# Optimization experiments

Measured on AMD Instinct MI355X. Metric: run time of the kernel, lower is better.

The kernel has to match this reference:

```python
import jax, jax.numpy as jnp
import numpy as np

EPS = 1e-5

def layer_norm(x, gamma, beta):
    mu = jnp.mean(x, axis=-1, keepdims=True)
    var = jnp.mean(jnp.square(x - mu), axis=-1, keepdims=True)
    return (x - mu) * jax.lax.rsqrt(var + EPS) * gamma + beta

def setup_inputs() -> dict:
    key = jax.random.key(0)
    ks = jax.random.split(key, 12)
    B, C, W, H = 4, 512, 48, 48
    HEADS, DH = 8, 64
    INNER = HEADS * DH  # 512
    CTX_D, CTX_L = 768, 77
    x = jax.random.normal(ks[0], (B, C, W, H), dtype=jnp.float32)
    context = jax.random.normal(ks[1], (B, CTX_L, CTX_D), dtype=jnp.float32)
    inv = lambda d: 1.0 / np.sqrt(d)
    return {
        'x': x,
        'context': context,
        'norm_gamma': jnp.ones((C,), jnp.float32),
        'null_kv': jax.random.normal(ks[2], (2, DH), dtype=jnp.float32),
        'Wq': jax.random.normal(ks[3], (C, INNER), dtype=jnp.float32) * inv(C),
        'Wkv': jax.random.normal(ks[4], (C, 2 * DH), dtype=jnp.float32) * inv(C),
        'ctx_ln_g': jnp.ones((CTX_D,), jnp.float32),
        'ctx_ln_b': jnp.zeros((CTX_D,), jnp.float32),
        'Wctx': jax.random.normal(ks[5], (CTX_D, 2 * DH), dtype=jnp.float32) * inv(CTX_D),
        'bctx': jnp.zeros((2 * DH,), jnp.float32),
        'Wout': jax.random.normal(ks[6], (INNER, C), dtype=jnp.float32) * inv(INNER),
        'out_ln_g': jnp.ones((C,), jnp.float32),
    }

def reference(x, context, norm_gamma, null_kv, Wq, Wkv, ctx_ln_g, ctx_ln_b, Wctx, bctx, Wout, out_ln_g):
    b, c, w, h = x.shape
    heads = 8
    dh = Wkv.shape[-1] // 2
    scale = dh ** -0.5
    # b c w h -> b (w h) c
    x_flat = jnp.transpose(x.reshape(b, c, w * h), (0, 2, 1))  # [b, n, c]
    xn = layer_norm(x_flat, norm_gamma, 0.0)
    q = xn @ Wq  # [b, n, heads*dh]
    kv = xn @ Wkv
    k, v = kv[..., :dh], kv[..., dh:]  # [b, n, dh]
    n = w * h
    q = q.reshape(b, n, heads, dh).transpose(0, 2, 1, 3) * scale  # [b, h, n, d]
    # null kv: [2, dh] -> broadcast to [b, 1, dh] each
    nk = jnp.broadcast_to(null_kv[0], (b, 1, dh))
    nv = jnp.broadcast_to(null_kv[1], (b, 1, dh))
    k = jnp.concatenate([nk, k], axis=-2)
    v = jnp.concatenate([nv, v], axis=-2)
    # context kv
    ckv = layer_norm(context, ctx_ln_g, ctx_ln_b) @ Wctx + bctx
    ck, cv = ckv[..., :dh], ckv[..., dh:]
    k = jnp.concatenate([ck, k], axis=-2)  # [b, j, d]
    v = jnp.concatenate([cv, v], axis=-2)
    sim = jnp.einsum('bhid,bjd->bhij', q, k)  # [b, h, n, j]
    attn = jax.nn.softmax(sim, axis=-1)
    out = jnp.einsum('bhij,bjd->bhid', attn, v)
    out = out.transpose(0, 2, 1, 3).reshape(b, n, heads * dh)  # b n (h d)
    out = layer_norm(out @ Wout, out_ln_g, 0.0)
    y = x_flat + out  # [b, n, c]
    return jnp.transpose(y, (0, 2, 1)).reshape(b, c, w, h)
```

## Files before the change

### kernel.cpp

```cpp
#include <hip/hip_runtime.h>

typedef __attribute__((ext_vector_type(8))) short bf16x8;
typedef __attribute__((ext_vector_type(4))) float f32x4;

#define LPAD 2432
#define LKV  2382
#define NSEQ 2304
#define CDIM 512
#define LPSZ (4 * NSEQ * 8)

__device__ __forceinline__ unsigned short f2bf(float f) {
  unsigned int u = __builtin_bit_cast(unsigned int, f);
  u += 0x7fffu + ((u >> 16) & 1u);
  return (unsigned short)(u >> 16);
}
__device__ __forceinline__ float bf2f(unsigned short s) {
  unsigned int u = ((unsigned int)s) << 16;
  return __builtin_bit_cast(float, u);
}
__device__ __forceinline__ f32x4 MFMA(bf16x8 a, bf16x8 b, f32x4 c) {
  return __builtin_amdgcn_mfma_f32_16x16x32_bf16(a, b, c, 0, 0, 0);
}
__device__ __forceinline__ void stage16(const unsigned short* g, unsigned short* l) {
  __builtin_amdgcn_global_load_lds((const __attribute__((address_space(1))) void*)g,
                                   (__attribute__((address_space(3))) void*)l, 16, 0, 0);
}
__device__ __forceinline__ unsigned int cvtpk(float a, float b) {
  unsigned int r;
  asm("v_cvt_pk_bf16_f32 %0, %1, %2" : "=v"(r) : "v"(a), "v"(b));
  return r;
}
__device__ __forceinline__ int Fj(int j) {
  return (j & ~31) | ((j & 15) << 1) | ((j >> 4) & 1);
}

__device__ __forceinline__ void tr_tile(const float* __restrict__ in,
                                        unsigned short* __restrict__ out,
                                        int K, int N, int tk, int tn, int t) {
  __shared__ float T[32][33];
  int r = t >> 5, c = t & 31;
#pragma unroll
  for (int p = 0; p < 4; p++) {
    int rr = r + p * 8;
    T[rr][c] = in[(size_t)(tk * 32 + rr) * N + tn * 32 + c];
  }
  __syncthreads();
#pragma unroll
  for (int p = 0; p < 4; p++) {
    int rr = r + p * 8;
    out[(size_t)(tn * 32 + rr) * K + tk * 32 + c] = f2bf(T[c][rr]);
  }
}

__global__ void k_prep(const float* __restrict__ Wq, const float* __restrict__ Wkv,
                       const float* __restrict__ Wctx, const float* __restrict__ Wout,
                       unsigned short* __restrict__ WqT, unsigned short* __restrict__ WkvT,
                       unsigned short* __restrict__ WctxT, unsigned short* __restrict__ WoutT) {
  int bid = blockIdx.x, t = threadIdx.x;
  if (bid < 256) {
    tr_tile(Wq, WqT, 512, 512, bid >> 4, bid & 15, t);
  } else if (bid < 320) {
    int q = bid - 256;
    tr_tile(Wkv, WkvT, 512, 128, q >> 2, q & 3, t);
  } else if (bid < 416) {
    int q = bid - 320;
    tr_tile(Wctx, WctxT, 768, 128, q >> 2, q & 3, t);
  } else {
    int q = bid - 416;
    tr_tile(Wout, WoutT, 512, 512, q >> 4, q & 15, t);
  }
}

__global__ void k_ln1(const float* __restrict__ x, const float* __restrict__ g,
                      unsigned short* __restrict__ xn) {
  int b = blockIdx.y;
  int i0 = blockIdx.x * 32;
  int t = threadIdx.x;
  int ii = t & 31, ci = t >> 5;
  const float* xb = x + (size_t)b * CDIM * NSEQ;
  float s = 0.f, s2 = 0.f;
  for (int c = ci; c < CDIM; c += 8) {
    float v = xb[(size_t)c * NSEQ + i0 + ii];
    s += v; s2 += v * v;
  }
  __shared__ float ls[8][32], ls2[8][32];
  __shared__ float lmu[32], lrs[32];
  __shared__ float Lt[32][65];
  ls[ci][ii] = s; ls2[ci][ii] = s2;
  __syncthreads();
  if (t < 32) {
    float a = 0.f, a2 = 0.f;
    for (int q = 0; q < 8; q++) { a += ls[q][t]; a2 += ls2[q][t]; }
    float mu = a * (1.0f / 512.0f);
    float var = a2 * (1.0f / 512.0f) - mu * mu;
    lmu[t] = mu; lrs[t] = rsqrtf(var + 1e-5f);
  }
  __syncthreads();
  float mu = lmu[ii], rs = lrs[ii];
  int rr = t >> 3, cl0 = (t & 7) * 8;
  for (int cb = 0; cb < 8; cb++) {
#pragma unroll
    for (int e = 0; e < 8; e++) {
      int cl = ci + 8 * e;
      int c = cb * 64 + cl;
      float v = xb[(size_t)c * NSEQ + i0 + ii];
      Lt[ii][cl] = (v - mu) * rs * g[c];
    }
    __syncthreads();
    union { unsigned int w4[4]; uint4 u; } pk;
#pragma unroll
    for (int m = 0; m < 4; m++)
      pk.w4[m] = cvtpk(Lt[rr][cl0 + 2 * m], Lt[rr][cl0 + 2 * m + 1]);
    *reinterpret_cast<uint4*>(xn + (size_t)(b * NSEQ + i0 + rr) * CDIM + cb * 64 + cl0) = pk.u;
    __syncthreads();
  }
}

__global__ void k_ctx(const float* __restrict__ ctx, const float* __restrict__ g,
                      const float* __restrict__ be, const unsigned short* __restrict__ WctxT,
                      const float* __restrict__ bctx, const float* __restrict__ null_kv,
                      unsigned short* __restrict__ kb, unsigned short* __restrict__ vt) {
  int b = blockIdx.y, j = blockIdx.x;
  int t = threadIdx.x;
  if (j == 77) {
    if (t < 64) kb[((size_t)b * LPAD + 77) * 64 + t] = f2bf(null_kv[t]);
    else vt[((size_t)b * 64 + (t - 64)) * LPAD + Fj(77)] = f2bf(null_kv[64 + (t - 64)]);
    return;
  }
  if (j > 77) {
    int jj = LKV + (j - 78);
    if (t < 64) kb[((size_t)b * LPAD + jj) * 64 + t] = 0;
    else vt[((size_t)b * 64 + (t - 64)) * LPAD + Fj(jj)] = 0;
    return;
  }
  __shared__ float row[768];
  __shared__ float red[4];
  const float* src = ctx + (size_t)(b * 77 + j) * 768;
  float s = 0.f, s2 = 0.f;
  for (int k = t; k < 768; k += 128) {
    float v = src[k];
    row[k] = v; s += v; s2 += v * v;
  }
  for (int o = 32; o; o >>= 1) { s += __shfl_xor(s, o); s2 += __shfl_xor(s2, o); }
  if ((t & 63) == 0) { red[(t >> 6) * 2] = s; red[(t >> 6) * 2 + 1] = s2; }
  __syncthreads();
  float S = red[0] + red[2], S2 = red[1] + red[3];
  float mu = S * (1.0f / 768.0f);
  float rs = rsqrtf(S2 * (1.0f / 768.0f) - mu * mu + 1e-5f);
  __syncthreads();
  for (int k = t; k < 768; k += 128) row[k] = (row[k] - mu) * rs * g[k] + be[k];
  __syncthreads();
  const uint4* w4 = reinterpret_cast<const uint4*>(WctxT + (size_t)t * 768);
  float acc = 0.f;
  for (int k8 = 0; k8 < 96; k8++) {
    union { uint4 u; unsigned short s[8]; } wv;
    wv.u = w4[k8];
#pragma unroll
    for (int e = 0; e < 8; e++) acc += row[k8 * 8 + e] * bf2f(wv.s[e]);
  }
  acc += bctx[t];
  if (t < 64) kb[((size_t)b * LPAD + j) * 64 + t] = f2bf(acc);
  else vt[((size_t)b * 64 + (t - 64)) * LPAD + Fj(j)] = f2bf(acc);
}

template <int MODE>
__global__ __launch_bounds__(256, 1) void k_gemm(
    const unsigned short* __restrict__ A, const unsigned short* __restrict__ BT0,
    const unsigned short* __restrict__ BT1, unsigned short* __restrict__ out_q,
    unsigned short* __restrict__ out_k, unsigned short* __restrict__ out_vt,
    unsigned short* __restrict__ out_proj) {
  int m0 = blockIdx.x * 128, n0 = blockIdx.y * 64;
  int t = threadIdx.x;
  int lane = t & 63, w = t >> 6;
  int wm = w >> 1, wn = w & 1;
  int G = lane >> 4, li = lane & 15, li7 = lane & 7;
  __shared__ __align__(16) unsigned short Al[2][8192];
  __shared__ __align__(16) unsigned short Bl[2][4096];
  const unsigned short* BT = (MODE == 0 && n0 >= 512) ? BT1 : BT0;
  int bn0 = (MODE == 0 && n0 >= 512) ? n0 - 512 : n0;

  f32x4 zero = {0.f, 0.f, 0.f, 0.f};
  f32x4 acc[4][2];
#pragma unroll
  for (int a = 0; a < 4; a++)
#pragma unroll
    for (int c = 0; c < 2; c++) acc[a][c] = zero;

#define STAGE_AB(buf, k0)                                                              \
  {                                                                                    \
    _Pragma("unroll") for (int p = 0; p < 4; p++) {                                    \
      int gA = p * 256 + t;                                                            \
      int ra = gA >> 3;                                                                \
      int ca = ((gA & 7) ^ (ra & 7)) * 8;                                              \
      stage16(A + (size_t)(m0 + ra) * 512 + (k0) + ca, &Al[buf][(p * 256 + w * 64) * 8]); \
    }                                                                                  \
    _Pragma("unroll") for (int p = 0; p < 2; p++) {                                    \
      int gB = p * 256 + t;                                                            \
      int rb = gB >> 3;                                                                \
      int cb = ((gB & 7) ^ (rb & 7)) * 8;                                              \
      stage16(BT + (size_t)(bn0 + rb) * 512 + (k0) + cb, &Bl[buf][(p * 256 + w * 64) * 8]); \
    }                                                                                  \
  }

  STAGE_AB(0, 0)
  __syncthreads();

  for (int u = 0; u < 8; u++) {
    int cur = u & 1, nxt = cur ^ 1;
    if (u < 7) STAGE_AB(nxt, (u + 1) * 64)
    const char* Ac = (const char*)Al[cur];
    const char* Bc = (const char*)Bl[cur];
#pragma unroll
    for (int ks = 0; ks < 2; ks++) {
      bf16x8 af[4], bfr[2];
#pragma unroll
      for (int f = 0; f < 4; f++)
        af[f] = *reinterpret_cast<const bf16x8*>(
            Ac + ((((wm * 64 + f * 16 + li) * 8) + ((ks * 4 + G) ^ li7)) << 4));
#pragma unroll
      for (int f = 0; f < 2; f++)
        bfr[f] = *reinterpret_cast<const bf16x8*>(
            Bc + ((((wn * 32 + f * 16 + li) * 8) + ((ks * 4 + G) ^ li7)) << 4));
#pragma unroll
      for (int fm = 0; fm < 4; fm++)
#pragma unroll
        for (int fn = 0; fn < 2; fn++)
          acc[fm][fn] = MFMA(af[fm], bfr[fn], acc[fm][fn]);
    }
    __syncthreads();
  }
#undef STAGE_AB

#pragma unroll
  for (int fm = 0; fm < 4; fm++)
#pragma unroll
    for (int fn = 0; fn < 2; fn++)
#pragma unroll
      for (int r = 0; r < 4; r++) {
        int row = m0 + wm * 64 + fm * 16 + G * 4 + r;
        int col = n0 + wn * 32 + fn * 16 + li;
        float v = acc[fm][fn][r];
        if (MODE == 0) {
          int b = row / NSEQ, i = row - b * NSEQ;
          if (col < 512) out_q[(size_t)row * 512 + col] = f2bf(v * 0.18033688011112042f);
          else if (col < 576) out_k[((size_t)b * LPAD + 78 + i) * 64 + (col - 512)] = f2bf(v);
          else out_vt[((size_t)b * 64 + (col - 576)) * LPAD + Fj(78 + i)] = f2bf(v);
        } else {
          out_proj[(size_t)row * 512 + col] = f2bf(v);
        }
      }
}

__global__ __launch_bounds__(256, 4) void k_attn(
    const unsigned short* __restrict__ q, const unsigned short* __restrict__ kbuf,
    const unsigned short* __restrict__ vt, unsigned short* __restrict__ pO0,
    unsigned short* __restrict__ pO1, unsigned short* __restrict__ pO2,
    unsigned short* __restrict__ pO3, unsigned short* __restrict__ lp) {
  int bx = blockIdx.x;
  int it = bx >> 2, sp = bx & 3;
  int hh = blockIdx.y, b = blockIdx.z;
  int i0 = it * 32;
  int t = threadIdx.x;
  int w = t >> 6, lane = t & 63;
  int G = lane >> 4, li = lane & 15, li7 = lane & 7;
  int swzV = (li ^ (li >> 2)) & 3;
  int h = hh * 4 + w;

  __shared__ __align__(16) unsigned short Kl[2][2048];
  __shared__ __align__(16) unsigned short Vl[2][2048];

  int rk = t >> 3;
  int ck = ((t & 7) ^ (rk & 7)) * 8;
  int rv = t >> 2;
  int cv = ((t & 3) ^ ((rv ^ (rv >> 2)) & 3)) * 8;

  const unsigned short* kbase = kbuf + (size_t)b * LPAD * 64;
  const unsigned short* vbase = vt + (size_t)b * 64 * LPAD;

  bf16x8 qf[2][2];
#pragma unroll
  for (int fi = 0; fi < 2; fi++)
#pragma unroll
    for (int ks = 0; ks < 2; ks++)
      qf[fi][ks] = *reinterpret_cast<const bf16x8*>(
          q + (size_t)(b * NSEQ + i0 + fi * 16 + li) * CDIM + h * 64 + ks * 32 + G * 8);

  int jt0 = sp * 19;

  {
    int j0 = jt0 * 32;
    stage16(kbase + (size_t)(j0 + rk) * 64 + ck, &Kl[0][w * 512]);
    stage16(vbase + (size_t)rv * LPAD + j0 + cv, &Vl[0][w * 512]);
  }

  f32x4 zero = {0.f, 0.f, 0.f, 0.f};
  f32x4 OT[4][2];
#pragma unroll
  for (int fd = 0; fd < 4; fd++)
#pragma unroll
    for (int fi = 0; fi < 2; fi++) OT[fd][fi] = zero;
  float l_[2] = {0.f, 0.f};

  __syncthreads();

  for (int u = 0; u < 19; u++) {
    int jt = jt0 + u;
    int cur = u & 1, nxt = cur ^ 1;
    int j0 = jt * 32;
    if (u + 1 < 19) {
      int j1 = j0 + 32;
      stage16(kbase + (size_t)(j1 + rk) * 64 + ck, &Kl[nxt][w * 512]);
      stage16(vbase + (size_t)rv * LPAD + j1 + cv, &Vl[nxt][w * 512]);
    }
    const char* Kc = (const char*)Kl[cur];
    const char* Vc = (const char*)Vl[cur];

    f32x4 S[2][2];
#pragma unroll
    for (int fj = 0; fj < 2; fj++) { S[fj][0] = zero; S[fj][1] = zero; }
#pragma unroll
    for (int ks = 0; ks < 2; ks++) {
      bf16x8 kf[2];
#pragma unroll
      for (int fj = 0; fj < 2; fj++)
        kf[fj] = *reinterpret_cast<const bf16x8*>(
            Kc + ((((fj * 16 + li) * 8) + ((ks * 4 + G) ^ li7)) << 4));
#pragma unroll
      for (int fj = 0; fj < 2; fj++)
#pragma unroll
        for (int fi = 0; fi < 2; fi++)
          S[fj][fi] = MFMA(kf[fj], qf[fi][ks], S[fj][fi]);
    }
    if (j0 + 32 > LKV) {
#pragma unroll
      for (int fj = 0; fj < 2; fj++)
#pragma unroll
        for (int r = 0; r < 4; r++) {
          int jg = j0 + fj * 16 + G * 4 + r;
          if (jg >= LKV) { S[fj][0][r] = -1e30f; S[fj][1][r] = -1e30f; }
        }
    }
    bf16x8 pf[2];
#pragma unroll
    for (int fi = 0; fi < 2; fi++) {
      float e[2][4];
#pragma unroll
      for (int fj = 0; fj < 2; fj++)
#pragma unroll
        for (int r = 0; r < 4; r++) e[fj][r] = __builtin_exp2f(S[fj][fi][r]);
      float s0 = (e[0][0] + e[0][1]) + (e[0][2] + e[0][3]);
      float s1 = (e[1][0] + e[1][1]) + (e[1][2] + e[1][3]);
      l_[fi] += s0 + s1;
      union { unsigned int w4[4]; bf16x8 v; } u2;
#pragma unroll
      for (int m = 0; m < 4; m++) u2.w4[m] = cvtpk(e[0][m], e[1][m]);
      pf[fi] = u2.v;
    }
#pragma unroll
    for (int fd = 0; fd < 4; fd++) {
      bf16x8 uv = *reinterpret_cast<const bf16x8*>(
          Vc + (((fd * 16 + li) * 4 + (G ^ swzV)) << 4));
#pragma unroll
      for (int fi = 0; fi < 2; fi++) OT[fd][fi] = MFMA(uv, pf[fi], OT[fd][fi]);
    }
    __syncthreads();
  }

  unsigned short* pO = (sp == 0) ? pO0 : (sp == 1) ? pO1 : (sp == 2) ? pO2 : pO3;
#pragma unroll
  for (int fi = 0; fi < 2; fi++) {
    l_[fi] += __shfl_xor(l_[fi], 16);
    l_[fi] += __shfl_xor(l_[fi], 32);
    int row = b * NSEQ + i0 + fi * 16 + li;
    if (G == 0) lp[sp * LPSZ + row * 8 + h] = f2bf(l_[fi]);
#pragma unroll
    for (int fd = 0; fd < 4; fd++) {
      union { unsigned int w2[2]; uint2 u2; } pk;
      pk.w2[0] = cvtpk(OT[fd][fi][0], OT[fd][fi][1]);
      pk.w2[1] = cvtpk(OT[fd][fi][2], OT[fd][fi][3]);
      *reinterpret_cast<uint2*>(pO + (size_t)row * CDIM + h * 64 + fd * 16 + G * 4) = pk.u2;
    }
  }
}

__global__ void k_merge(unsigned short* __restrict__ pO0,
                        const unsigned short* __restrict__ pO1,
                        const unsigned short* __restrict__ pO2,
                        const unsigned short* __restrict__ pO3,
                        const unsigned short* __restrict__ lp) {
  int c = blockIdx.x * 256 + threadIdx.x;
  size_t base = (size_t)c * 8;
  int row = (int)(base >> 9);
  int h = (int)((base >> 6) & 7);
  int li = row * 8 + h;
  float l = bf2f(lp[li]) + bf2f(lp[LPSZ + li]) + bf2f(lp[2 * LPSZ + li]) + bf2f(lp[3 * LPSZ + li]);
  float inv = 1.0f / l;
  union { uint4 u; unsigned short s[8]; } a0, a1, a2, a3, o;
  a0.u = *reinterpret_cast<const uint4*>(pO0 + base);
  a1.u = *reinterpret_cast<const uint4*>(pO1 + base);
  a2.u = *reinterpret_cast<const uint4*>(pO2 + base);
  a3.u = *reinterpret_cast<const uint4*>(pO3 + base);
  unsigned int* ow = reinterpret_cast<unsigned int*>(&o.u);
#pragma unroll
  for (int m = 0; m < 4; m++) {
    float v0 = (bf2f(a0.s[2 * m]) + bf2f(a1.s[2 * m]) + bf2f(a2.s[2 * m]) + bf2f(a3.s[2 * m])) * inv;
    float v1 = (bf2f(a0.s[2 * m + 1]) + bf2f(a1.s[2 * m + 1]) + bf2f(a2.s[2 * m + 1]) +
                bf2f(a3.s[2 * m + 1])) * inv;
    ow[m] = cvtpk(v0, v1);
  }
  *reinterpret_cast<uint4*>(pO0 + base) = o.u;
}

__global__ void k_stats(const unsigned short* __restrict__ proj, float* __restrict__ musig) {
  int w = threadIdx.x >> 6, lane = threadIdx.x & 63;
  int row = blockIdx.x * 4 + w;
  union { uint4 u; unsigned short s[8]; } a;
  a.u = *reinterpret_cast<const uint4*>(proj + (size_t)row * CDIM + lane * 8);
  float s = 0.f, s2 = 0.f;
#pragma unroll
  for (int m = 0; m < 8; m++) {
    float v = bf2f(a.s[m]);
    s += v; s2 += v * v;
  }
  for (int o = 32; o; o >>= 1) { s += __shfl_xor(s, o); s2 += __shfl_xor(s2, o); }
  if (lane == 0) {
    float mu = s * (1.0f / 512.0f);
    float var = s2 * (1.0f / 512.0f) - mu * mu;
    musig[row] = mu;
    musig[4 * NSEQ + row] = rsqrtf(var + 1e-5f);
  }
}

__global__ void k_final2(const unsigned short* __restrict__ proj, const float* __restrict__ musig,
                         const float* __restrict__ g, const float* __restrict__ x,
                         float* __restrict__ y) {
  int i0 = blockIdx.x * 32, c0 = blockIdx.y * 64, b = blockIdx.z;
  int t = threadIdx.x;
  __shared__ float lds[32][65];
  {
    int il = t >> 3, cB = (t & 7) * 8;
    union { uint4 u; unsigned short s[8]; } a;
    a.u = *reinterpret_cast<const uint4*>(proj + (size_t)(b * NSEQ + i0 + il) * CDIM + c0 + cB);
#pragma unroll
    for (int m = 0; m < 8; m++) lds[il][cB + m] = bf2f(a.s[m]);
  }
  __syncthreads();
  int ii = t & 31, cg = t >> 5;
  float mu = musig[b * NSEQ + i0 + ii];
  float rs = musig[4 * NSEQ + b * NSEQ + i0 + ii];
  const float* xb = x + (size_t)b * CDIM * NSEQ;
  float* yb = y + (size_t)b * CDIM * NSEQ;
#pragma unroll
  for (int cc = 0; cc < 8; cc++) {
    int cl = cg * 8 + cc;
    int c = c0 + cl;
    float v = lds[ii][cl];
    yb[(size_t)c * NSEQ + i0 + ii] = xb[(size_t)c * NSEQ + i0 + ii] + (v - mu) * rs * g[c];
  }
}

extern "C" void kernel_launch(void* const* d_in, const int* in_sizes, int n_in,
                              void* d_out, int out_size, void* d_ws, size_t ws_size,
                              hipStream_t stream) {
  const float* x       = (const float*)d_in[0];
  const float* context = (const float*)d_in[1];
  const float* ngamma  = (const float*)d_in[2];
  const float* null_kv = (const float*)d_in[3];
  const float* Wq      = (const float*)d_in[4];
  const float* Wkv     = (const float*)d_in[5];
  const float* clng    = (const float*)d_in[6];
  const float* clnb    = (const float*)d_in[7];
  const float* Wctx    = (const float*)d_in[8];
  const float* bctx    = (const float*)d_in[9];
  const float* Wout    = (const float*)d_in[10];
  const float* olng    = (const float*)d_in[11];
  float* y = (float*)d_out;
  char* ws = (char*)d_ws;

  unsigned short* xn    = (unsigned short*)(ws);
  unsigned short* qb    = (unsigned short*)(ws + 9437184);
  unsigned short* proj  = (unsigned short*)(ws);
  unsigned short* aoutb = (unsigned short*)(ws + 18874368);
  float* musig          = (float*)(ws + 18874368);
  unsigned short* kb    = (unsigned short*)(ws + 28311552);
  unsigned short* vtb   = (unsigned short*)(ws + 29556736);
  unsigned short* WqT   = (unsigned short*)(ws + 30801920);
  unsigned short* WkvT  = (unsigned short*)(ws + 31326208);
  unsigned short* WctxT = (unsigned short*)(ws + 31457280);
  unsigned short* WoutT = (unsigned short*)(ws + 31653888);
  unsigned short* lpart = (unsigned short*)(ws + 30801920);
  unsigned short* pO2   = (unsigned short*)d_out;
  unsigned short* pO3   = (unsigned short*)d_out + 4718592;

  k_prep<<<dim3(672), dim3(256), 0, stream>>>(Wq, Wkv, Wctx, Wout, WqT, WkvT, WctxT, WoutT);
  k_ln1<<<dim3(72, 4), dim3(256), 0, stream>>>(x, ngamma, xn);
  k_ctx<<<dim3(128, 4), dim3(128), 0, stream>>>(context, clng, clnb, WctxT, bctx, null_kv, kb, vtb);
  k_gemm<0><<<dim3(72, 10), dim3(256), 0, stream>>>(xn, WqT, WkvT, qb, kb, vtb, nullptr);
  k_attn<<<dim3(288, 2, 4), dim3(256), 0, stream>>>(qb, kb, vtb, aoutb, xn, pO2, pO3, lpart);
  k_merge<<<dim3(2304), dim3(256), 0, stream>>>(aoutb, xn, pO2, pO3, lpart);
  k_gemm<1><<<dim3(72, 8), dim3(256), 0, stream>>>(aoutb, WoutT, nullptr, nullptr, nullptr, nullptr, proj);
  k_stats<<<dim3(2304), dim3(256), 0, stream>>>(proj, musig);
  k_final2<<<dim3(72, 8, 4), dim3(256), 0, stream>>>(proj, musig, olng, x, y);
}
```

Measured before the change: 168.5 us.

## Split attention KV range into three chunks and cache LN1 input in LDS

New measurement: 167.9 us. About the same (-0.4%).

```diff
diff --git a/kernel.cpp b/kernel.cpp
--- a/kernel.cpp
+++ b/kernel.cpp
@@ -78,14 +78,15 @@
   int t = threadIdx.x;
   int ii = t & 31, ci = t >> 5;
   const float* xb = x + (size_t)b * CDIM * NSEQ;
+  __shared__ unsigned short Xs[32][514];
+  __shared__ float ls[8][32], ls2[8][32];
+  __shared__ float lmu[32], lrs[32];
   float s = 0.f, s2 = 0.f;
   for (int c = ci; c < CDIM; c += 8) {
     float v = xb[(size_t)c * NSEQ + i0 + ii];
+    Xs[ii][c] = f2bf(v);
     s += v; s2 += v * v;
   }
-  __shared__ float ls[8][32], ls2[8][32];
-  __shared__ float lmu[32], lrs[32];
-  __shared__ float Lt[32][65];
   ls[ci][ii] = s; ls2[ci][ii] = s2;
   __syncthreads();
   if (t < 32) {
@@ -96,23 +97,20 @@
     lmu[t] = mu; lrs[t] = rsqrtf(var + 1e-5f);
   }
   __syncthreads();
-  float mu = lmu[ii], rs = lrs[ii];
   int rr = t >> 3, cl0 = (t & 7) * 8;
+  float mu = lmu[rr], rs = lrs[rr];
+  unsigned short* xrow = xn + (size_t)(b * NSEQ + i0 + rr) * CDIM;
+#pragma unroll
   for (int cb = 0; cb < 8; cb++) {
-#pragma unroll
-    for (int e = 0; e < 8; e++) {
-      int cl = ci + 8 * e;
-      int c = cb * 64 + cl;
-      float v = xb[(size_t)c * NSEQ + i0 + ii];
-      Lt[ii][cl] = (v - mu) * rs * g[c];
-    }
-    __syncthreads();
+    int c0 = cb * 64 + cl0;
     union { unsigned int w4[4]; uint4 u; } pk;
 #pragma unroll
-    for (int m = 0; m < 4; m++)
-      pk.w4[m] = cvtpk(Lt[rr][cl0 + 2 * m], Lt[rr][cl0 + 2 * m + 1]);
-    *reinterpret_cast<uint4*>(xn + (size_t)(b * NSEQ + i0 + rr) * CDIM + cb * 64 + cl0) = pk.u;
-    __syncthreads();
+    for (int m = 0; m < 4; m++) {
+      float v0 = (bf2f(Xs[rr][c0 + 2 * m]) - mu) * rs * g[c0 + 2 * m];
+      float v1 = (bf2f(Xs[rr][c0 + 2 * m + 1]) - mu) * rs * g[c0 + 2 * m + 1];
+      pk.w4[m] = cvtpk(v0, v1);
+    }
+    *reinterpret_cast<uint4*>(xrow + c0) = pk.u;
   }
 }
 
@@ -255,10 +253,11 @@
     const unsigned short* __restrict__ q, const unsigned short* __restrict__ kbuf,
     const unsigned short* __restrict__ vt, unsigned short* __restrict__ pO0,
     unsigned short* __restrict__ pO1, unsigned short* __restrict__ pO2,
-    unsigned short* __restrict__ pO3, unsigned short* __restrict__ lp) {
-  int bx = blockIdx.x;
-  int it = bx >> 2, sp = bx & 3;
-  int hh = blockIdx.y, b = blockIdx.z;
+    unsigned short* __restrict__ lp) {
+  int it = blockIdx.x;
+  int yy = blockIdx.y;
+  int sp = yy >> 1, hh = yy & 1;
+  int b = blockIdx.z;
   int i0 = it * 32;
   int t = threadIdx.x;
   int w = t >> 6, lane = t & 63;
@@ -285,7 +284,8 @@
       qf[fi][ks] = *reinterpret_cast<const bf16x8*>(
           q + (size_t)(b * NSEQ + i0 + fi * 16 + li) * CDIM + h * 64 + ks * 32 + G * 8);
 
-  int jt0 = sp * 19;
+  int jt0 = sp * 25;
+  int nt = (sp == 2) ? 26 : 25;
 
   {
     int j0 = jt0 * 32;
@@ -303,11 +303,11 @@
 
   __syncthreads();
 
-  for (int u = 0; u < 19; u++) {
+  for (int u = 0; u < nt; u++) {
     int jt = jt0 + u;
     int cur = u & 1, nxt = cur ^ 1;
     int j0 = jt * 32;
-    if (u + 1 < 19) {
+    if (u + 1 < nt) {
       int j1 = j0 + 32;
       stage16(kbase + (size_t)(j1 + rk) * 64 + ck, &Kl[nxt][w * 512]);
       stage16(vbase + (size_t)rv * LPAD + j1 + cv, &Vl[nxt][w * 512]);
@@ -366,7 +366,7 @@
     __syncthreads();
   }
 
-  unsigned short* pO = (sp == 0) ? pO0 : (sp == 1) ? pO1 : (sp == 2) ? pO2 : pO3;
+  unsigned short* pO = (sp == 0) ? pO0 : (sp == 1) ? pO1 : pO2;
 #pragma unroll
   for (int fi = 0; fi < 2; fi++) {
     l_[fi] += __shfl_xor(l_[fi], 16);
@@ -386,26 +386,23 @@
 __global__ void k_merge(unsigned short* __restrict__ pO0,
                         const unsigned short* __restrict__ pO1,
                         const unsigned short* __restrict__ pO2,
-                        const unsigned short* __restrict__ pO3,
                         const unsigned short* __restrict__ lp) {
   int c = blockIdx.x * 256 + threadIdx.x;
   size_t base = (size_t)c * 8;
   int row = (int)(base >> 9);
   int h = (int)((base >> 6) & 7);
   int li = row * 8 + h;
-  float l = bf2f(lp[li]) + bf2f(lp[LPSZ + li]) + bf2f(lp[2 * LPSZ + li]) + bf2f(lp[3 * LPSZ + li]);
+  float l = bf2f(lp[li]) + bf2f(lp[LPSZ + li]) + bf2f(lp[2 * LPSZ + li]);
   float inv = 1.0f / l;
-  union { uint4 u; unsigned short s[8]; } a0, a1, a2, a3, o;
+  union { uint4 u; unsigned short s[8]; } a0, a1, a2, o;
   a0.u = *reinterpret_cast<const uint4*>(pO0 + base);
   a1.u = *reinterpret_cast<const uint4*>(pO1 + base);
   a2.u = *reinterpret_cast<const uint4*>(pO2 + base);
-  a3.u = *reinterpret_cast<const uint4*>(pO3 + base);
   unsigned int* ow = reinterpret_cast<unsigned int*>(&o.u);
 #pragma unroll
   for (int m = 0; m < 4; m++) {
-    float v0 = (bf2f(a0.s[2 * m]) + bf2f(a1.s[2 * m]) + bf2f(a2.s[2 * m]) + bf2f(a3.s[2 * m])) * inv;
-    float v1 = (bf2f(a0.s[2 * m + 1]) + bf2f(a1.s[2 * m + 1]) + bf2f(a2.s[2 * m + 1]) +
-                bf2f(a3.s[2 * m + 1])) * inv;
+    float v0 = (bf2f(a0.s[2 * m]) + bf2f(a1.s[2 * m]) + bf2f(a2.s[2 * m])) * inv;
+    float v1 = (bf2f(a0.s[2 * m + 1]) + bf2f(a1.s[2 * m + 1]) + bf2f(a2.s[2 * m + 1])) * inv;
     ow[m] = cvtpk(v0, v1);
   }
   *reinterpret_cast<uint4*>(pO0 + base) = o.u;
@@ -490,14 +487,13 @@
   unsigned short* WoutT = (unsigned short*)(ws + 31653888);
   unsigned short* lpart = (unsigned short*)(ws + 30801920);
   unsigned short* pO2   = (unsigned short*)d_out;
-  unsigned short* pO3   = (unsigned short*)d_out + 4718592;
 
   k_prep<<<dim3(672), dim3(256), 0, stream>>>(Wq, Wkv, Wctx, Wout, WqT, WkvT, WctxT, WoutT);
   k_ln1<<<dim3(72, 4), dim3(256), 0, stream>>>(x, ngamma, xn);
   k_ctx<<<dim3(128, 4), dim3(128), 0, stream>>>(context, clng, clnb, WctxT, bctx, null_kv, kb, vtb);
   k_gemm<0><<<dim3(72, 10), dim3(256), 0, stream>>>(xn, WqT, WkvT, qb, kb, vtb, nullptr);
-  k_attn<<<dim3(288, 2, 4), dim3(256), 0, stream>>>(qb, kb, vtb, aoutb, xn, pO2, pO3, lpart);
-  k_merge<<<dim3(2304), dim3(256), 0, stream>>>(aoutb, xn, pO2, pO3, lpart);
+  k_attn<<<dim3(72, 6, 4), dim3(256), 0, stream>>>(qb, kb, vtb, aoutb, xn, pO2, lpart);
+  k_merge<<<dim3(2304), dim3(256), 0, stream>>>(aoutb, xn, pO2, lpart);
   k_gemm<1><<<dim3(72, 8), dim3(256), 0, stream>>>(aoutb, WoutT, nullptr, nullptr, nullptr, nullptr, proj);
   k_stats<<<dim3(2304), dim3(256), 0, stream>>>(proj, musig);
   k_final2<<<dim3(72, 8, 4), dim3(256), 0, stream>>>(proj, musig, olng, x, y);
```

## Cache LN1 input in LDS and read attention V straight from global

Applied to the files above, without the earlier changes.

After: 412.4 us. +144.8%, slower.

```diff
diff --git a/kernel.cpp b/kernel.cpp
--- a/kernel.cpp
+++ b/kernel.cpp
@@ -78,14 +78,15 @@
   int t = threadIdx.x;
   int ii = t & 31, ci = t >> 5;
   const float* xb = x + (size_t)b * CDIM * NSEQ;
+  __shared__ unsigned short Xs[32][514];
+  __shared__ float ls[8][32], ls2[8][32];
+  __shared__ float lmu[32], lrs[32];
   float s = 0.f, s2 = 0.f;
   for (int c = ci; c < CDIM; c += 8) {
     float v = xb[(size_t)c * NSEQ + i0 + ii];
+    Xs[ii][c] = f2bf(v);
     s += v; s2 += v * v;
   }
-  __shared__ float ls[8][32], ls2[8][32];
-  __shared__ float lmu[32], lrs[32];
-  __shared__ float Lt[32][65];
   ls[ci][ii] = s; ls2[ci][ii] = s2;
   __syncthreads();
   if (t < 32) {
@@ -96,23 +97,20 @@
     lmu[t] = mu; lrs[t] = rsqrtf(var + 1e-5f);
   }
   __syncthreads();
-  float mu = lmu[ii], rs = lrs[ii];
   int rr = t >> 3, cl0 = (t & 7) * 8;
+  float mu = lmu[rr], rs = lrs[rr];
+  unsigned short* xrow = xn + (size_t)(b * NSEQ + i0 + rr) * CDIM;
+#pragma unroll
   for (int cb = 0; cb < 8; cb++) {
-#pragma unroll
-    for (int e = 0; e < 8; e++) {
-      int cl = ci + 8 * e;
-      int c = cb * 64 + cl;
-      float v = xb[(size_t)c * NSEQ + i0 + ii];
-      Lt[ii][cl] = (v - mu) * rs * g[c];
-    }
-    __syncthreads();
+    int c0 = cb * 64 + cl0;
     union { unsigned int w4[4]; uint4 u; } pk;
 #pragma unroll
-    for (int m = 0; m < 4; m++)
-      pk.w4[m] = cvtpk(Lt[rr][cl0 + 2 * m], Lt[rr][cl0 + 2 * m + 1]);
-    *reinterpret_cast<uint4*>(xn + (size_t)(b * NSEQ + i0 + rr) * CDIM + cb * 64 + cl0) = pk.u;
-    __syncthreads();
+    for (int m = 0; m < 4; m++) {
+      float v0 = (bf2f(Xs[rr][c0 + 2 * m]) - mu) * rs * g[c0 + 2 * m];
+      float v1 = (bf2f(Xs[rr][c0 + 2 * m + 1]) - mu) * rs * g[c0 + 2 * m + 1];
+      pk.w4[m] = cvtpk(v0, v1);
+    }
+    *reinterpret_cast<uint4*>(xrow + c0) = pk.u;
   }
 }
 
@@ -251,7 +249,7 @@
       }
 }
 
-__global__ __launch_bounds__(256, 4) void k_attn(
+__global__ __launch_bounds__(256, 8) void k_attn(
     const unsigned short* __restrict__ q, const unsigned short* __restrict__ kbuf,
     const unsigned short* __restrict__ vt, unsigned short* __restrict__ pO0,
     unsigned short* __restrict__ pO1, unsigned short* __restrict__ pO2,
@@ -263,19 +261,15 @@
   int t = threadIdx.x;
   int w = t >> 6, lane = t & 63;
   int G = lane >> 4, li = lane & 15, li7 = lane & 7;
-  int swzV = (li ^ (li >> 2)) & 3;
   int h = hh * 4 + w;
 
   __shared__ __align__(16) unsigned short Kl[2][2048];
-  __shared__ __align__(16) unsigned short Vl[2][2048];
 
   int rk = t >> 3;
   int ck = ((t & 7) ^ (rk & 7)) * 8;
-  int rv = t >> 2;
-  int cv = ((t & 3) ^ ((rv ^ (rv >> 2)) & 3)) * 8;
 
   const unsigned short* kbase = kbuf + (size_t)b * LPAD * 64;
-  const unsigned short* vbase = vt + (size_t)b * 64 * LPAD;
+  const unsigned short* vrow = vt + ((size_t)b * 64 + li) * LPAD + G * 8;
 
   bf16x8 qf[2][2];
 #pragma unroll
@@ -287,11 +281,7 @@
 
   int jt0 = sp * 19;
 
-  {
-    int j0 = jt0 * 32;
-    stage16(kbase + (size_t)(j0 + rk) * 64 + ck, &Kl[0][w * 512]);
-    stage16(vbase + (size_t)rv * LPAD + j0 + cv, &Vl[0][w * 512]);
-  }
+  stage16(kbase + (size_t)(jt0 * 32 + rk) * 64 + ck, &Kl[0][w * 512]);
 
   f32x4 zero = {0.f, 0.f, 0.f, 0.f};
   f32x4 OT[4][2];
@@ -307,13 +297,9 @@
     int jt = jt0 + u;
     int cur = u & 1, nxt = cur ^ 1;
     int j0 = jt * 32;
-    if (u + 1 < 19) {
-      int j1 = j0 + 32;
-      stage16(kbase + (size_t)(j1 + rk) * 64 + ck, &Kl[nxt][w * 512]);
-      stage16(vbase + (size_t)rv * LPAD + j1 + cv, &Vl[nxt][w * 512]);
-    }
+    if (u + 1 < 19)
+      stage16(kbase + (size_t)(j0 + 32 + rk) * 64 + ck, &Kl[nxt][w * 512]);
     const char* Kc = (const char*)Kl[cur];
-    const char* Vc = (const char*)Vl[cur];
 
     f32x4 S[2][2];
 #pragma unroll
@@ -358,8 +344,7 @@
     }
 #pragma unroll
     for (int fd = 0; fd < 4; fd++) {
-      bf16x8 uv = *reinterpret_cast<const bf16x8*>(
-          Vc + (((fd * 16 + li) * 4 + (G ^ swzV)) << 4));
+      bf16x8 uv = *reinterpret_cast<const bf16x8*>(vrow + (size_t)(fd * 16) * LPAD + j0);
 #pragma unroll
       for (int fi = 0; fi < 2; fi++) OT[fd][fi] = MFMA(uv, pf[fi], OT[fd][fi]);
     }
```
